# Performance work log

Hardware: AMD Instinct MI355X
Metric: run time of the kernel (lower is better)

Reference implementation:

```python
import jax, jax.numpy as jnp
import numpy as np

N = 50000
E = 400000
IN_DIM = 256
H1, D1 = 4, 128   # gat1: heads=4, hidden=128, concat -> 512
H2, D2 = 1, 64    # gat2: heads=1, out=64, concat=False
NEG_SLOPE = 0.2


def setup_inputs() -> dict:
    key = jax.random.key(0)
    ks = jax.random.split(key, 12)
    x = jax.random.normal(ks[0], (N, IN_DIM), dtype=jnp.float32)
    edge_index = jax.random.randint(ks[1], (2, E), 0, N, dtype=jnp.int64)
    edge_attr = jax.random.normal(ks[2], (E,), dtype=jnp.float32)
    # Glorot-ish init for weights, zeros for biases (as in PyG GATConv)
    def glorot(k, shape):
        fan = shape[0] + shape[-1]
        return jax.random.normal(k, shape, dtype=jnp.float32) * jnp.sqrt(2.0 / fan)
    W1 = glorot(ks[3], (IN_DIM, H1 * D1))
    a1_src = glorot(ks[4], (H1, D1))
    a1_dst = glorot(ks[5], (H1, D1))
    b1 = jnp.zeros((H1 * D1,), dtype=jnp.float32)
    W2 = glorot(ks[6], (H1 * D1, H2 * D2))
    a2_src = glorot(ks[7], (H2, D2))
    a2_dst = glorot(ks[8], (H2, D2))
    b2 = jnp.zeros((D2,), dtype=jnp.float32)
    return {"x": x, "edge_index": edge_index, "edge_attr": edge_attr,
            "W1": W1, "a1_src": a1_src, "a1_dst": a1_dst, "b1": b1,
            "W2": W2, "a2_src": a2_src, "a2_dst": a2_dst, "b2": b2}


def _gat_layer(x, src, dst, W, a_s, a_d, b, heads, d, concat):
    n = x.shape[0]
    h = (x @ W).reshape(n, heads, d)                      # [N,H,D]
    alpha_s = jnp.einsum('nhd,hd->nh', h, a_s)            # [N,H]
    alpha_d = jnp.einsum('nhd,hd->nh', h, a_d)
    e = jax.nn.leaky_relu(alpha_s[src] + alpha_d[dst], NEG_SLOPE)  # [Etot,H]
    # segment softmax over incoming edges of each dst node
    emax = jax.ops.segment_max(e, dst, num_segments=n)
    ex = jnp.exp(e - emax[dst])
    denom = jax.ops.segment_sum(ex, dst, num_segments=n)
    alpha = ex / (denom[dst] + 1e-16)                     # [Etot,H]
    msg = h[src] * alpha[:, :, None]                      # [Etot,H,D]
    out = jax.ops.segment_sum(msg, dst, num_segments=n)   # [N,H,D]
    out = out.reshape(n, heads * d) if concat else out.mean(axis=1)
    return out + b


def reference(x, edge_index, edge_attr, W1, a1_src, a1_dst, b1,
              W2, a2_src, a2_dst, b2):
    # edge_attr is ignored (GATConv built without edge_dim)
    loop = jnp.arange(N, dtype=edge_index.dtype)          # PyG add_self_loops=True
    src = jnp.concatenate([edge_index[0], loop])
    dst = jnp.concatenate([edge_index[1], loop])
    h = _gat_layer(x, src, dst, W1, a1_src, a1_dst, b1, H1, D1, True)
    h = jax.nn.elu(h)
    out = _gat_layer(h, src, dst, W2, a2_src, a2_dst, b2, H2, D2, False)
    return out
```

## Files before the change

### kernel.cpp

```cpp
#include <hip/hip_runtime.h>
#include <cstdint>

typedef unsigned short u16;
typedef short bf16x8_t __attribute__((ext_vector_type(8)));
typedef float f32x4_t __attribute__((ext_vector_type(4)));

#define DEVFN __device__ __forceinline__

DEVFN u16 f2bf(float f) {
  unsigned u = __builtin_bit_cast(unsigned, f);
  u = (u + 0x7fffu + ((u >> 16) & 1u)) >> 16;
  return (u16)u;
}
DEVFN float bf2f(u16 s) {
  unsigned u = ((unsigned)s) << 16;
  return __builtin_bit_cast(float, u);
}
DEVFN unsigned pk2bf(float a, float b) {
  return (unsigned)f2bf(a) | ((unsigned)f2bf(b) << 16);
}

DEVFN void gload_lds16(const u16* g, u16* l) {
  __builtin_amdgcn_global_load_lds(
      (const __attribute__((address_space(1))) void*)g,
      (__attribute__((address_space(3))) void*)l, 16, 0, 0);
}

__global__ void prep_kernel(const float* __restrict__ W1, const float* __restrict__ W2,
                            const float* __restrict__ a1s, const float* __restrict__ a1d,
                            const int* __restrict__ edst,
                            u16* __restrict__ w1t, u16* __restrict__ w2t,
                            float* __restrict__ ws1, float* __restrict__ wd1,
                            int* __restrict__ cnt, int e) {
  int b = blockIdx.x;
  if (b < 512) {
    int idx = b * 256 + threadIdx.x;
    int k = idx >> 9, m = idx & 511;
    w1t[m * 256 + k] = f2bf(W1[idx]);
  } else if (b < 640) {
    int idx = (b - 512) * 256 + threadIdx.x;
    int k = idx >> 6, m = idx & 63;
    w2t[m * 512 + k] = f2bf(W2[idx]);
  } else if (b < 648) {
    int b2 = b - 640;
    int h = b2 >> 1;
    int isD = b2 & 1;
    const float* av = (isD ? a1d : a1s) + h * 128;
    int k = threadIdx.x;
    float sum = 0.f;
#pragma unroll 8
    for (int d = 0; d < 128; ++d)
      sum = fmaf(W1[k * 512 + h * 128 + d], av[d], sum);
    (isD ? wd1 : ws1)[h * 256 + k] = sum;
  } else {
    int i = (b - 648) * 256 + threadIdx.x;
    if (i < e) atomicAdd(&cnt[edst[i]], 1);
  }
}

__global__ __launch_bounds__(256) void conv_alpha_kernel(
    const float* __restrict__ x, const float* __restrict__ ws1, const float* __restrict__ wd1,
    u16* __restrict__ xb, float* __restrict__ as1, float* __restrict__ ad1, int n)
{
  int node = (blockIdx.x * 256 + threadIdx.x) >> 6;
  int lane = threadIdx.x & 63;
  if (node >= n) return;
  float4 xv = *reinterpret_cast<const float4*>(x + (size_t)node * 256 + lane * 4);
  uint2 pk;
  pk.x = pk2bf(xv.x, xv.y);
  pk.y = pk2bf(xv.z, xv.w);
  *reinterpret_cast<uint2*>(xb + (size_t)node * 256 + lane * 4) = pk;

  float p[8];
#pragma unroll
  for (int v = 0; v < 8; ++v) {
    const float* wv = (v < 4 ? ws1 : wd1) + (v & 3) * 256 + lane * 4;
    float4 w4 = *reinterpret_cast<const float4*>(wv);
    p[v] = xv.x * w4.x + xv.y * w4.y + xv.z * w4.z + xv.w * w4.w;
  }
#pragma unroll
  for (int d = 1; d < 64; d <<= 1) {
#pragma unroll
    for (int v = 0; v < 8; ++v) p[v] += __shfl_xor(p[v], d, 64);
  }
  if (lane == 0) {
    *reinterpret_cast<float4*>(as1 + (size_t)node * 4) = make_float4(p[0], p[1], p[2], p[3]);
    *reinterpret_cast<float4*>(ad1 + (size_t)node * 4) = make_float4(p[4], p[5], p[6], p[7]);
  }
}

DEVFN int block_scan_256(int v, int tid, int* wsum) {
#pragma unroll
  for (int d = 1; d < 64; d <<= 1) {
    int u = __shfl_up(v, d, 64);
    if ((tid & 63) >= d) v += u;
  }
  if ((tid & 63) == 63) wsum[tid >> 6] = v;
  __syncthreads();
  int add = 0;
#pragma unroll
  for (int w = 0; w < 4; ++w) add += (w < (tid >> 6)) ? wsum[w] : 0;
  __syncthreads();
  return v + add;
}

__global__ __launch_bounds__(256) void scan_a_kernel(const int* __restrict__ cnt, int* __restrict__ bsum, int n) {
  __shared__ int ws4[4];
  int i = blockIdx.x * 256 + threadIdx.x;
  int v = (i < n) ? cnt[i] + 1 : 0;
  int incl = block_scan_256(v, threadIdx.x, ws4);
  if (threadIdx.x == 255) bsum[blockIdx.x] = incl;
}

__global__ __launch_bounds__(256) void scan_c_kernel(
    const int* __restrict__ cnt, const int* __restrict__ bsum,
    int* __restrict__ rowoff, int* __restrict__ cursor, int n)
{
  __shared__ int ws4[4];
  __shared__ int ws4b[4];
  __shared__ int base_sh;
  int pre = 0;
  for (int w = threadIdx.x; w < blockIdx.x; w += 256) pre += bsum[w];
#pragma unroll
  for (int d = 1; d < 64; d <<= 1) pre += __shfl_xor(pre, d, 64);
  if ((threadIdx.x & 63) == 0) ws4b[threadIdx.x >> 6] = pre;
  __syncthreads();
  if (threadIdx.x == 0) base_sh = ws4b[0] + ws4b[1] + ws4b[2] + ws4b[3];
  int i = blockIdx.x * 256 + threadIdx.x;
  int v = (i < n) ? cnt[i] + 1 : 0;
  int incl = block_scan_256(v, threadIdx.x, ws4);
  int off = base_sh + incl - v;
  if (i < n) {
    rowoff[i] = off;
    cursor[i] = off;
    if (i == n - 1) rowoff[n] = off + v;
  }
}

__global__ void scatter_kernel(const int* __restrict__ srcs, const int* __restrict__ dsts,
                               int* __restrict__ cursor, int* __restrict__ csr, int e, int n) {
  int i = blockIdx.x * 256 + threadIdx.x;
  if (i >= e + n) return;
  int s, d;
  if (i < e) { s = srcs[i]; d = dsts[i]; }
  else       { s = i - e; d = s; }
  int pos = atomicAdd(&cursor[d], 1);
  csr[pos] = s;
}

__global__ __launch_bounds__(256) void aggx_kernel(
    const u16* __restrict__ xb, const float* __restrict__ as1,
    const float* __restrict__ ad1, const int* __restrict__ rowoff,
    const int* __restrict__ csr, u16* __restrict__ aggx, size_t plane, int n)
{
  int node = (blockIdx.x * 256 + threadIdx.x) >> 6;
  int lane = threadIdx.x & 63;
  if (node >= n) return;
  int e0 = rowoff[node], e1 = rowoff[node + 1];
  float4 adv = *reinterpret_cast<const float4*>(ad1 + (size_t)node * 4);
  const unsigned dimb = (unsigned)lane * 4;

  float acc[4][4];
#pragma unroll
  for (int h = 0; h < 4; ++h)
#pragma unroll
    for (int d = 0; d < 4; ++d) acc[h][d] = 0.f;
  float den[4] = {0.f, 0.f, 0.f, 0.f};

  for (int e = e0; e < e1; ++e) {
    unsigned s = (unsigned)csr[e];
    float4 a4 = *reinterpret_cast<const float4*>(as1 + ((size_t)s << 2));
    float ex[4];
    {
      float t0 = a4.x + adv.x, t1 = a4.y + adv.y, t2 = a4.z + adv.z, t3 = a4.w + adv.w;
      ex[0] = __expf(fmaxf(t0, 0.2f * t0));
      ex[1] = __expf(fmaxf(t1, 0.2f * t1));
      ex[2] = __expf(fmaxf(t2, 0.2f * t2));
      ex[3] = __expf(fmaxf(t3, 0.2f * t3));
    }
#pragma unroll
    for (int h = 0; h < 4; ++h) den[h] += ex[h];
    uint2 xv = *reinterpret_cast<const uint2*>(xb + (((size_t)s << 8) + dimb));
    float xf[4];
    xf[0] = bf2f((u16)(xv.x & 0xffffu));
    xf[1] = bf2f((u16)(xv.x >> 16));
    xf[2] = bf2f((u16)(xv.y & 0xffffu));
    xf[3] = bf2f((u16)(xv.y >> 16));
#pragma unroll
    for (int h = 0; h < 4; ++h)
#pragma unroll
      for (int d = 0; d < 4; ++d) acc[h][d] = fmaf(ex[h], xf[d], acc[h][d]);
  }

#pragma unroll
  for (int h = 0; h < 4; ++h) {
    float inv = 1.f / (den[h] + 1e-16f);
    uint2 o;
    o.x = pk2bf(acc[h][0] * inv, acc[h][1] * inv);
    o.y = pk2bf(acc[h][2] * inv, acc[h][3] * inv);
    *reinterpret_cast<uint2*>(aggx + (size_t)h * plane + ((size_t)node << 8) + dimb) = o;
  }
}


template<int BM, int BN, int WROWS, int K, int BK>
__global__ __launch_bounds__(256) void gemm1_kernel(
    const u16* __restrict__ Aall, const u16* __restrict__ BT,
    const float* __restrict__ b1, u16* __restrict__ C, int M, size_t plane)
{
  constexpr int WM = BM / WROWS;
  constexpr int MF = WM / 16;
  constexpr int NF = BN / 16;
  constexpr int KK = BK / 32;
  static_assert(BK == 64, "swizzle derived for 128B rows");
  __shared__ __align__(16) u16 sA[BM][BK];
  __shared__ __align__(16) u16 sB[BN][BK];

  const int tid = threadIdx.x;
  const int lane = tid & 63;
  const int wr = tid >> 6;
  const int brow = blockIdx.x * BM;
  const int bcol = blockIdx.y * BN;
  const u16* A = Aall + blockIdx.y * plane;

  f32x4_t acc[MF][NF];
#pragma unroll
  for (int i = 0; i < MF; ++i)
#pragma unroll
    for (int j = 0; j < NF; ++j) acc[i][j] = f32x4_t{0.f, 0.f, 0.f, 0.f};

  const int rsel = lane & 15;
  const int kgrp = (lane >> 4) * 8;
  const int rx = (rsel & 7) * 8;

#pragma unroll
  for (int k0 = 0; k0 < K; k0 += BK) {
    constexpr int RA = BM * BK / 2048;
#pragma unroll
    for (int c = 0; c < RA; ++c) {
      int t = c * 256 + tid;
      int row = t >> 3;
      int col = ((t & 7) ^ (row & 7)) * 8;
      int gr = brow + row; gr = gr < M ? gr : M - 1;
      gload_lds16(A + (size_t)gr * K + k0 + col, &sA[0][0] + t * 8);
    }
    constexpr int RB = BN * BK / 2048;
#pragma unroll
    for (int c = 0; c < RB; ++c) {
      int t = c * 256 + tid;
      int row = t >> 3;
      int col = ((t & 7) ^ (row & 7)) * 8;
      gload_lds16(BT + (size_t)(bcol + row) * K + k0 + col, &sB[0][0] + t * 8);
    }
    __syncthreads();
#pragma unroll
    for (int kk = 0; kk < KK; ++kk) {
      const int cswz = (kk * 32 + kgrp) ^ rx;
      bf16x8_t af[MF], bfr[NF];
#pragma unroll
      for (int i = 0; i < MF; ++i) {
        int row = wr * WM + i * 16 + rsel;
        af[i] = *reinterpret_cast<const bf16x8_t*>(&sA[0][0] + row * BK + cswz);
      }
#pragma unroll
      for (int j = 0; j < NF; ++j) {
        int row = j * 16 + rsel;
        bfr[j] = *reinterpret_cast<const bf16x8_t*>(&sB[0][0] + row * BK + cswz);
      }
#pragma unroll
      for (int i = 0; i < MF; ++i)
#pragma unroll
        for (int j = 0; j < NF; ++j)
          acc[i][j] = __builtin_amdgcn_mfma_f32_16x16x32_bf16(af[i], bfr[j], acc[i][j], 0, 0, 0);
    }
    __syncthreads();
  }

  const int crow0 = (lane >> 4) * 4;
  const int ccol = lane & 15;
#pragma unroll
  for (int i = 0; i < MF; ++i)
#pragma unroll
    for (int j = 0; j < NF; ++j)
#pragma unroll
      for (int rr = 0; rr < 4; ++rr) {
        int gr = brow + wr * WM + i * 16 + crow0 + rr;
        int gc = bcol + j * 16 + ccol;
        if (gr < M) {
          float v = acc[i][j][rr] + b1[gc];
          v = v > 0.f ? v : expm1f(v);
          C[(size_t)gr * 512 + gc] = f2bf(v);
        }
      }
}

template<int BM, int BN, int WROWS, int K, int BK, int H, int DH>
__global__ __launch_bounds__(256) void gemm_alpha_kernel(
    const u16* __restrict__ A, const u16* __restrict__ BT, u16* __restrict__ C,
    const float* __restrict__ a_s, const float* __restrict__ a_d,
    float* __restrict__ as_out, float* __restrict__ ad_out, int M, int N)
{
  static_assert(BN == DH, "alpha store ownership");
  static_assert(BK == 64, "swizzle derived for 128B rows");
  constexpr int WM = BM / WROWS;
  constexpr int MF = WM / 16;
  constexpr int NF = BN / 16;
  constexpr int KK = BK / 32;
  __shared__ __align__(16) u16 sA[BM][BK];
  __shared__ __align__(16) u16 sB[BN][BK];

  const int tid = threadIdx.x;
  const int lane = tid & 63;
  const int wr = tid >> 6;
  const int brow = blockIdx.x * BM;
  const int bcol = blockIdx.y * BN;

  f32x4_t acc[MF][NF];
#pragma unroll
  for (int i = 0; i < MF; ++i)
#pragma unroll
    for (int j = 0; j < NF; ++j) acc[i][j] = f32x4_t{0.f, 0.f, 0.f, 0.f};

  const int rsel = lane & 15;
  const int kgrp = (lane >> 4) * 8;
  const int rx = (rsel & 7) * 8;

#pragma unroll
  for (int k0 = 0; k0 < K; k0 += BK) {
    constexpr int RA = BM * BK / 2048;
#pragma unroll
    for (int c = 0; c < RA; ++c) {
      int t = c * 256 + tid;
      int row = t >> 3;
      int col = ((t & 7) ^ (row & 7)) * 8;
      int gr = brow + row; gr = gr < M ? gr : M - 1;
      gload_lds16(A + (size_t)gr * K + k0 + col, &sA[0][0] + t * 8);
    }
    constexpr int RB = BN * BK / 2048;
#pragma unroll
    for (int c = 0; c < RB; ++c) {
      int t = c * 256 + tid;
      int row = t >> 3;
      int col = ((t & 7) ^ (row & 7)) * 8;
      gload_lds16(BT + (size_t)(bcol + row) * K + k0 + col, &sB[0][0] + t * 8);
    }
    __syncthreads();
#pragma unroll
    for (int kk = 0; kk < KK; ++kk) {
      const int cswz = (kk * 32 + kgrp) ^ rx;
      bf16x8_t af[MF], bfr[NF];
#pragma unroll
      for (int i = 0; i < MF; ++i) {
        int row = wr * WM + i * 16 + rsel;
        af[i] = *reinterpret_cast<const bf16x8_t*>(&sA[0][0] + row * BK + cswz);
      }
#pragma unroll
      for (int j = 0; j < NF; ++j) {
        int row = j * 16 + rsel;
        bfr[j] = *reinterpret_cast<const bf16x8_t*>(&sB[0][0] + row * BK + cswz);
      }
#pragma unroll
      for (int i = 0; i < MF; ++i)
#pragma unroll
        for (int j = 0; j < NF; ++j)
          acc[i][j] = __builtin_amdgcn_mfma_f32_16x16x32_bf16(af[i], bfr[j], acc[i][j], 0, 0, 0);
    }
    __syncthreads();
  }

  const int crow0 = (lane >> 4) * 4;
  const int ccol = lane & 15;

#pragma unroll
  for (int i = 0; i < MF; ++i)
#pragma unroll
    for (int j = 0; j < NF; ++j)
#pragma unroll
      for (int rr = 0; rr < 4; ++rr) {
        int gr = brow + wr * WM + i * 16 + crow0 + rr;
        int gc = bcol + j * 16 + ccol;
        if (gr < M) C[(size_t)gr * N + gc] = f2bf(acc[i][j][rr]);
      }

  const int head = bcol / DH;
  float asv[NF], adv[NF];
#pragma unroll
  for (int j = 0; j < NF; ++j) {
    int gc = bcol + j * 16 + ccol;
    asv[j] = a_s[gc];
    adv[j] = a_d[gc];
  }
#pragma unroll
  for (int i = 0; i < MF; ++i) {
#pragma unroll
    for (int rr = 0; rr < 4; ++rr) {
      float ps = 0.f, pd = 0.f;
#pragma unroll
      for (int j = 0; j < NF; ++j) {
        float v = acc[i][j][rr];
        ps = fmaf(v, asv[j], ps);
        pd = fmaf(v, adv[j], pd);
      }
#pragma unroll
      for (int d = 1; d < 16; d <<= 1) {
        ps += __shfl_xor(ps, d, 64);
        pd += __shfl_xor(pd, d, 64);
      }
      if ((lane & 15) == 0) {
        int gr = brow + wr * WM + i * 16 + crow0 + rr;
        if (gr < M) {
          as_out[(size_t)gr * H + head] = ps;
          ad_out[(size_t)gr * H + head] = pd;
        }
      }
    }
  }
}

__global__ __launch_bounds__(256) void agg2_kernel(
    const u16* __restrict__ h2, const float* __restrict__ as2,
    const float* __restrict__ ad2, const int* __restrict__ rowoff,
    const int* __restrict__ csr, const float* __restrict__ b2,
    float* __restrict__ out, int n)
{
  int node = (blockIdx.x * 256 + threadIdx.x) >> 5;
  int l32 = threadIdx.x & 31;
  if (node >= n) return;
  int e0 = rowoff[node], e1 = rowoff[node + 1];
  float advn = ad2[node];

  float acc0 = 0.f, acc1 = 0.f, den = 0.f;
  for (int e = e0; e < e1; ++e) {
    unsigned s = (unsigned)csr[e];
    float t = as2[s] + advn;
    float l = fmaxf(t, 0.2f * t);
    float ex = __expf(l);
    den += ex;
    unsigned hv = *reinterpret_cast<const unsigned*>(h2 + (s << 6) + l32 * 2);
    acc0 = fmaf(ex, bf2f((u16)(hv & 0xffffu)), acc0);
    acc1 = fmaf(ex, bf2f((u16)(hv >> 16)), acc1);
  }
  float inv = 1.f / (den + 1e-16f);
  float2 o;
  o.x = acc0 * inv + b2[l32 * 2];
  o.y = acc1 * inv + b2[l32 * 2 + 1];
  *reinterpret_cast<float2*>(out + (((size_t)node) << 6) + l32 * 2) = o;
}

extern "C" void kernel_launch(void* const* d_in, const int* in_sizes, int n_in,
                              void* d_out, int out_size, void* d_ws, size_t ws_size,
                              hipStream_t stream) {
  const float* x   = (const float*)d_in[0];
  const int*   ei  = (const int*)d_in[1];
  const float* W1  = (const float*)d_in[3];
  const float* a1s = (const float*)d_in[4];
  const float* a1d = (const float*)d_in[5];
  const float* b1  = (const float*)d_in[6];
  const float* W2  = (const float*)d_in[7];
  const float* a2s = (const float*)d_in[8];
  const float* a2d = (const float*)d_in[9];
  const float* b2  = (const float*)d_in[10];
  float* out = (float*)d_out;

  const int IN_DIM = 256, H1D1 = 512, D2 = 64;
  const int N = in_sizes[0] / IN_DIM;
  const int E = in_sizes[1] / 2;

  char* ws = (char*)d_ws;
  size_t off = 0;
  auto alloc = [&](size_t bytes) -> void* {
    void* p = ws + off;
    off += (bytes + 255) & ~(size_t)255;
    return p;
  };
  u16*  w1t    = (u16*)alloc((size_t)H1D1 * IN_DIM * 2);
  u16*  w2t    = (u16*)alloc((size_t)D2 * H1D1 * 2);
  float* ws1   = (float*)alloc(4 * 256 * 4);
  float* wd1   = (float*)alloc(4 * 256 * 4);
  u16*  xb     = (u16*)alloc((size_t)N * IN_DIM * 2);
  float* as1   = (float*)alloc((size_t)N * 4 * 4);
  float* ad1   = (float*)alloc((size_t)N * 4 * 4);
  int*  cnt    = (int*)alloc((size_t)N * 4);
  int*  cursor = (int*)alloc((size_t)N * 4);
  int*  rowoff = (int*)alloc((size_t)(N + 1) * 4);
  int*  bsum   = (int*)alloc(256 * 4);
  int*  csr    = (int*)alloc((size_t)(E + N) * 4);
  size_t plane = (size_t)N * IN_DIM;
  u16*  aggx   = (u16*)alloc(4 * plane * 2);
  u16*  h1o    = (u16*)alloc((size_t)N * H1D1 * 2);
  (void)n_in; (void)out_size; (void)ws_size;

  u16*   h2b = xb;
  float* as2 = (float*)(xb + (size_t)N * D2);
  float* ad2 = as2 + N;

  const int* esrc = ei;
  const int* edst = ei + E;

  (void)hipMemsetAsync(cnt, 0, (size_t)N * 4, stream);

  int eb = (E + 255) / 256;
  prep_kernel<<<648 + eb, 256, 0, stream>>>(W1, W2, a1s, a1d, edst, w1t, w2t, ws1, wd1, cnt, E);

  conv_alpha_kernel<<<(N + 3) / 4, 256, 0, stream>>>(x, ws1, wd1, xb, as1, ad1, N);

  int nsb = (N + 255) / 256;
  scan_a_kernel<<<nsb, 256, 0, stream>>>(cnt, bsum, N);
  scan_c_kernel<<<nsb, 256, 0, stream>>>(cnt, bsum, rowoff, cursor, N);
  scatter_kernel<<<(E + N + 255) / 256, 256, 0, stream>>>(esrc, edst, cursor, csr, E, N);

  aggx_kernel<<<(N + 3) / 4, 256, 0, stream>>>(xb, as1, ad1, rowoff, csr, aggx, plane, N);

  dim3 g1((N + 127) / 128, 4);
  gemm1_kernel<128, 128, 4, 256, 64><<<g1, 256, 0, stream>>>(aggx, w1t, b1, h1o, N, plane);

  dim3 g2((N + 63) / 64, 1);
  gemm_alpha_kernel<64, 64, 4, 512, 64, 1, 64><<<g2, 256, 0, stream>>>(
      h1o, w2t, h2b, a2s, a2d, as2, ad2, N, D2);

  agg2_kernel<<<((size_t)N * 32 + 255) / 256, 256, 0, stream>>>(h2b, as2, ad2, rowoff, csr, b2, out, N);
}
```

Baseline: 265.0 us.

## Remap gemm1 blocks per XCD, stage A via registers, use fast exp in ELU

Flattens gemm1's grid to 1D and remaps block IDs so that the four column blocks (heads) of each row block land on the same XCD. This is meant to improve L2 reuse of the A tile. It also replaces the direct global-to-LDS loads of A with register loads followed by swizzled LDS stores, and swaps expm1f for __expf(v)-1 in the ELU epilogue. The register staging adds VGPR pressure and extra LDS store instructions, and __expf-1 loses precision near zero.

```diff
diff --git a/kernel.cpp b/kernel.cpp
--- a/kernel.cpp
+++ b/kernel.cpp
@@ -202,8 +202,7 @@
   }
 }
 
-
-template<int BM, int BN, int WROWS, int K, int BK>
+template<int BM, int BN, int WROWS, int K, int BK, int NP>
 __global__ __launch_bounds__(256) void gemm1_kernel(
     const u16* __restrict__ Aall, const u16* __restrict__ BT,
     const float* __restrict__ b1, u16* __restrict__ C, int M, size_t plane)
@@ -219,9 +218,18 @@
   const int tid = threadIdx.x;
   const int lane = tid & 63;
   const int wr = tid >> 6;
-  const int brow = blockIdx.x * BM;
-  const int bcol = blockIdx.y * BN;
-  const u16* A = Aall + blockIdx.y * plane;
+
+  const int bid = blockIdx.x;
+  const int xcd = bid & 7;
+  const int rest = bid >> 3;
+  const int p = rest & (NP - 1);
+  const int rb = rest / NP;
+  const int r = rb * 8 + xcd;
+  const int NRB = (M + BM - 1) / BM;
+  if (r >= NRB) return;
+  const int brow = r * BM;
+  const int bcol = p * BN;
+  const u16* A = Aall + (size_t)p * plane;
 
   f32x4_t acc[MF][NF];
 #pragma unroll
@@ -236,13 +244,20 @@
 #pragma unroll
   for (int k0 = 0; k0 < K; k0 += BK) {
     constexpr int RA = BM * BK / 2048;
+    bf16x8_t av[RA];
 #pragma unroll
     for (int c = 0; c < RA; ++c) {
       int t = c * 256 + tid;
       int row = t >> 3;
-      int col = ((t & 7) ^ (row & 7)) * 8;
       int gr = brow + row; gr = gr < M ? gr : M - 1;
-      gload_lds16(A + (size_t)gr * K + k0 + col, &sA[0][0] + t * 8);
+      av[c] = *reinterpret_cast<const bf16x8_t*>(A + (size_t)gr * K + k0 + (t & 7) * 8);
+    }
+#pragma unroll
+    for (int c = 0; c < RA; ++c) {
+      int t = c * 256 + tid;
+      int row = t >> 3;
+      int slot = (t & 7) ^ (row & 7);
+      *reinterpret_cast<bf16x8_t*>(&sA[0][0] + row * BK + slot * 8) = av[c];
     }
     constexpr int RB = BN * BK / 2048;
 #pragma unroll
@@ -288,7 +303,7 @@
         int gc = bcol + j * 16 + ccol;
         if (gr < M) {
           float v = acc[i][j][rr] + b1[gc];
-          v = v > 0.f ? v : expm1f(v);
+          v = v > 0.f ? v : (__expf(v) - 1.0f);
           C[(size_t)gr * 512 + gc] = f2bf(v);
         }
       }
@@ -511,8 +526,9 @@
 
   aggx_kernel<<<(N + 3) / 4, 256, 0, stream>>>(xb, as1, ad1, rowoff, csr, aggx, plane, N);
 
-  dim3 g1((N + 127) / 128, 4);
-  gemm1_kernel<128, 128, 4, 256, 64><<<g1, 256, 0, stream>>>(aggx, w1t, b1, h1o, N, plane);
+  const int NRB = (N + 127) / 128;
+  const int g1 = ((NRB + 7) / 8) * 8 * 4;
+  gemm1_kernel<128, 128, 4, 256, 64, 4><<<g1, 256, 0, stream>>>(aggx, w1t, b1, h1o, N, plane);
 
   dim3 g2((N + 63) / 64, 1);
   gemm_alpha_kernel<64, 64, 4, 512, 64, 1, 64><<<g2, 256, 0, stream>>>(
```

New measurement: 255.5 us. -3.6%, faster.
